# Optimization experiments

Hardware: AMD Instinct MI355X
Metric: run time of the kernel (lower is better)

Reference implementation:

```python
import jax, jax.numpy as jnp
import numpy as np

MP1, NX, P, HT, HE = 524288, 32768, 128, 128, 64


def setup_inputs() -> dict:
    key = jax.random.key(0)
    ks = jax.random.split(key, 12)
    w = lambda k, shape, fan_in: jax.random.normal(k, shape, jnp.float32) / np.sqrt(fan_in).astype(np.float32)
    a = jax.random.normal(ks[0], (MP1,), jnp.float32)
    x = jax.random.uniform(ks[1], (NX,), jnp.float32)
    t = jax.random.uniform(ks[2], (), jnp.float32)
    # DeepONet-style operator net: branch Linear(Mp1 -> p), trunk MLP (x,t) -> p
    Wb = w(ks[3], (P, MP1), MP1); bb = jnp.zeros((P,), jnp.float32)
    Wt1 = w(ks[4], (HT, 2), 2); bt1 = jnp.zeros((HT,), jnp.float32)
    Wt2 = w(ks[5], (HT, HT), HT); bt2 = jnp.zeros((HT,), jnp.float32)
    Wt3 = w(ks[6], (P, HT), HT); bt3 = jnp.zeros((P,), jnp.float32)
    # EnergyNet F(y,z): tiny smooth MLP R^2 -> R (needs 3rd-order derivatives)
    We1 = w(ks[7], (HE, 2), 2); be1 = jnp.zeros((HE,), jnp.float32)
    We2 = w(ks[8], (HE, HE), HE); be2 = jnp.zeros((HE,), jnp.float32)
    We3 = w(ks[9], (1, HE), HE); be3 = jnp.zeros((1,), jnp.float32)
    return dict(a=a, x=x, t=t, Wb=Wb, bb=bb, Wt1=Wt1, bt1=bt1, Wt2=Wt2, bt2=bt2,
                Wt3=Wt3, bt3=bt3, We1=We1, be1=be1, We2=We2, be2=be2, We3=We3, be3=be3)


def reference(a, x, t, Wb, bb, Wt1, bt1, Wt2, bt2, Wt3, bt3, We1, be1, We2, be2, We3, be3):
    # branch encoding of the input function a: (P,)
    b = Wb @ a + bb

    def u_fn(xi):  # scalar x -> scalar u(x, t)
        h = jnp.tanh(Wt1 @ jnp.stack([xi, t]) + bt1)
        h = jnp.tanh(Wt2 @ h + bt2)
        return jnp.dot(b, Wt3 @ h + bt3)

    def F(y, z):  # EnergyNet: scalar (y, z) -> scalar
        h = jnp.tanh(We1 @ jnp.stack([y, z]) + be1)
        h = jnp.tanh(We2 @ h + be2)
        return (We3 @ h + be3)[0]

    # u and its spatial derivatives, vmapped over the Nx grid points
    u = jax.vmap(u_fn)(x)
    u_x = jax.vmap(jax.grad(u_fn))(x)
    u_xx = jax.vmap(jax.grad(jax.grad(u_fn)))(x)
    u_xxx = jax.vmap(jax.grad(jax.grad(jax.grad(u_fn))))(x)

    # all needed partials of F(y, z), exactly as in the original module
    F_y = jax.grad(F)
    F_yz = jax.vmap(jax.grad(F_y, 1))(u, u_x)
    F_yy, F_yyz = jax.vmap(jax.value_and_grad(jax.grad(F_y), 1))(u, u_x)
    F_zz, (F_yzz, F_zzz) = jax.vmap(jax.value_and_grad(jax.grad(jax.grad(F, 1), 1), (0, 1)))(u, u_x)

    F_yx = F_yy * u_x + F_yz * u_xx
    F_zxx = (F_yz * u_xx + F_zz * u_xxx + F_yyz * u_x ** 2
             + 2.0 * F_yzz * u_x * u_xx + F_zzz * u_xx ** 2)
    return (-F_yx + F_zxx).reshape(x.shape[0])
```

## Files before the change

kernel.cpp:

```cpp
#include <hip/hip_runtime.h>
#include <cmath>

#define MP1 524288
#define NXP 32768


__global__ __launch_bounds__(256) void prep1_k(const float* __restrict__ Wt2,
                                               const float* __restrict__ We2,
                                               float* __restrict__ ws) {
    int idx = blockIdx.x * 256 + threadIdx.x;
    if (idx < 128) ws[idx] = 0.0f;
    if (idx < 16384) {
        int j = idx >> 7, k = idx & 127;
        ws[512 + k * 128 + j] = Wt2[idx];
    }
    if (idx < 4096) {
        int m = idx >> 6, i = idx & 63;
        ws[16896 + i * 64 + m] = We2[idx];
    }
}

__global__ __launch_bounds__(256) void gemv_k(const float* __restrict__ Wb,
                                              const float* __restrict__ a,
                                              float* __restrict__ b_acc) {
    const int row = blockIdx.y;
    const int chunk = blockIdx.x;
    const int t = threadIdx.x;
    size_t base = (size_t)row * MP1 + (size_t)chunk * 16384;
    const float4* W4 = (const float4*)(Wb + base);
    const float4* A4 = (const float4*)(a + (size_t)chunk * 16384);
    float sum = 0.0f;
#pragma unroll
    for (int it = 0; it < 16; ++it) {
        float4 w = W4[t + it * 256];
        float4 av = A4[t + it * 256];
        sum += w.x * av.x + w.y * av.y + w.z * av.z + w.w * av.w;
    }
#pragma unroll
    for (int off = 32; off > 0; off >>= 1) sum += __shfl_down(sum, off, 64);
    __shared__ float red[4];
    int wid = t >> 6;
    if ((t & 63) == 0) red[wid] = sum;
    __syncthreads();
    if (t == 0) atomicAdd(&b_acc[row], red[0] + red[1] + red[2] + red[3]);
}

__global__ __launch_bounds__(128) void prep2_k(const float* __restrict__ ws_in,
                                               const float* __restrict__ bb,
                                               const float* __restrict__ Wt3,
                                               const float* __restrict__ bt3,
                                               float* __restrict__ ws) {
    int k = threadIdx.x;
    float cv = 0.0f;
    for (int j = 0; j < 128; ++j)
        cv = fmaf(ws_in[j] + bb[j], Wt3[j * 128 + k], cv);
    ws[128 + k] = cv;
    float p = (ws_in[k] + bb[k]) * bt3[k];
#pragma unroll
    for (int off = 32; off > 0; off >>= 1) p += __shfl_down(p, off, 64);
    __shared__ float red[2];
    if ((k & 63) == 0) red[k >> 6] = p;
    __syncthreads();
    if (k == 0) ws[256] = red[0] + red[1];
}

#define H1V 0
#define RED 8192
#define URED 10240
#define FRED 10496
#define LDSF 13568

__global__ __launch_bounds__(512, 4) void point_k(const float* __restrict__ x,
                                                  const float* __restrict__ tptr,
                                                  const float* __restrict__ Wt1,
                                                  const float* __restrict__ bt1,
                                                  const float* __restrict__ bt2,
                                                  const float* __restrict__ We1,
                                                  const float* __restrict__ be1,
                                                  const float* __restrict__ be2,
                                                  const float* __restrict__ We3,
                                                  const float* __restrict__ ws,
                                                  float* __restrict__ out) {
    __shared__ float lds[LDSF];
    const int tid = threadIdx.x;
    const int p = tid & 63;
    const int slice = __builtin_amdgcn_readfirstlane(tid >> 6);
    const int i = blockIdx.x * 64 + p;
    const float xi = x[i];
    const float tt = tptr[0];
    const float* __restrict__ cvec = ws + 128;
    const float* __restrict__ WT2t = ws + 512;
    const float* __restrict__ WE2t = ws + 16896;
    const float u_const = ws[256];

#pragma unroll
    for (int q = 0; q < 16; ++q) {
        int k = slice * 16 + q;
        float z = fmaf(Wt1[2 * k], xi, fmaf(Wt1[2 * k + 1], tt, bt1[k]));
        lds[H1V + k * 64 + p] = tanhf(z);
    }
    __syncthreads();

    {
        float a0[16], a1[16], a2[16], a3[16];
#pragma unroll
        for (int jj = 0; jj < 16; ++jj) { a0[jj] = 0.f; a1[jj] = 0.f; a2[jj] = 0.f; a3[jj] = 0.f; }
#pragma unroll 2
        for (int k = 0; k < 128; ++k) {
            float v = lds[H1V + k * 64 + p];
            float w = Wt1[2 * k];
            float s = 1.f - v * v;
            float f2 = -2.f * v * s;
            float f3 = 2.f * s * (2.f * v * v - s);
            float d1 = s * w;
            float d2 = f2 * w * w;
            float d3 = f3 * w * w * w;
            const float* wrow = WT2t + k * 128 + slice * 16;
#pragma unroll
            for (int jj = 0; jj < 16; ++jj) {
                float wjk = wrow[jj];
                a0[jj] = fmaf(wjk, v, a0[jj]);
                a1[jj] = fmaf(wjk, d1, a1[jj]);
                a2[jj] = fmaf(wjk, d2, a2[jj]);
                a3[jj] = fmaf(wjk, d3, a3[jj]);
            }
        }
        float u0 = 0.f, u1 = 0.f, u2 = 0.f, u3 = 0.f;
#pragma unroll
        for (int jj = 0; jj < 16; ++jj) {
            int j = slice * 16 + jj;
            float z0 = a0[jj] + bt2[j];
            float z1 = a1[jj], z2 = a2[jj], z3 = a3[jj];
            float v = tanhf(z0);
            float s = 1.f - v * v;
            float f2 = -2.f * v * s;
            float f3 = 2.f * s * (2.f * v * v - s);
            float cj = cvec[j];
            u0 = fmaf(cj, v, u0);
            u1 = fmaf(cj, s * z1, u1);
            u2 = fmaf(cj, f2 * z1 * z1 + s * z2, u2);
            u3 = fmaf(cj, f3 * z1 * z1 * z1 + 3.f * f2 * z1 * z2 + s * z3, u3);
        }
        float* r = lds + RED + (slice * 64 + p) * 4;
        r[0] = u0; r[1] = u1; r[2] = u2; r[3] = u3;
    }
    __syncthreads();

    if (tid < 64) {
        float u0 = u_const, u1 = 0.f, u2 = 0.f, u3 = 0.f;
#pragma unroll
        for (int s = 0; s < 8; ++s) {
            const float* r = lds + RED + (s * 64 + tid) * 4;
            u0 += r[0]; u1 += r[1]; u2 += r[2]; u3 += r[3];
        }
        float* u = lds + URED + tid * 4;
        u[0] = u0; u[1] = u1; u[2] = u2; u[3] = u3;
    }
    __syncthreads();

    const float y = lds[URED + p * 4 + 0];
    const float z = lds[URED + p * 4 + 1];

#pragma unroll
    for (int q = 0; q < 8; ++q) {
        int ii = slice * 8 + q;
        float g = fmaf(We1[2 * ii], y, fmaf(We1[2 * ii + 1], z, be1[ii]));
        lds[H1V + ii * 64 + p] = tanhf(g);
    }
    __syncthreads();

    {
        float A0[8], A1[8], A2[8], A3[8], A4[8], A5[8], A6[8], A7[8], A8[8];
#pragma unroll
        for (int mm = 0; mm < 8; ++mm) {
            A0[mm] = 0.f; A1[mm] = 0.f; A2[mm] = 0.f; A3[mm] = 0.f; A4[mm] = 0.f;
            A5[mm] = 0.f; A6[mm] = 0.f; A7[mm] = 0.f; A8[mm] = 0.f;
        }
#pragma unroll 2
        for (int ii = 0; ii < 64; ++ii) {
            float v = lds[H1V + ii * 64 + p];
            float w0 = We1[2 * ii], w1 = We1[2 * ii + 1];
            float s = 1.f - v * v;
            float f2 = -2.f * v * s;
            float f3 = 2.f * s * (2.f * v * v - s);
            float j1 = s * w0, j2 = s * w1;
            float j3 = f2 * w0 * w0, j4 = f2 * w0 * w1, j5 = f2 * w1 * w1;
            float j6 = f3 * w0 * w0 * w1, j7 = f3 * w0 * w1 * w1, j8 = f3 * w1 * w1 * w1;
            const float* wrow = WE2t + ii * 64 + slice * 8;
#pragma unroll
            for (int mm = 0; mm < 8; ++mm) {
                float wmi = wrow[mm];
                A0[mm] = fmaf(wmi, v,  A0[mm]);
                A1[mm] = fmaf(wmi, j1, A1[mm]);
                A2[mm] = fmaf(wmi, j2, A2[mm]);
                A3[mm] = fmaf(wmi, j3, A3[mm]);
                A4[mm] = fmaf(wmi, j4, A4[mm]);
                A5[mm] = fmaf(wmi, j5, A5[mm]);
                A6[mm] = fmaf(wmi, j6, A6[mm]);
                A7[mm] = fmaf(wmi, j7, A7[mm]);
                A8[mm] = fmaf(wmi, j8, A8[mm]);
            }
        }
        float Fyy = 0.f, Fyz = 0.f, Fzz = 0.f, Fyyz = 0.f, Fyzz = 0.f, Fzzz = 0.f;
#pragma unroll
        for (int mm = 0; mm < 8; ++mm) {
            int m = slice * 8 + mm;
            float G0 = A0[mm] + be2[m];
            float v = tanhf(G0);
            float s = 1.f - v * v;
            float f2 = -2.f * v * s;
            float f3 = 2.f * s * (2.f * v * v - s);
            float Gy = A1[mm], Gz = A2[mm];
            float Gyy = A3[mm], Gyz = A4[mm], Gzz = A5[mm];
            float Hyy = f2 * Gy * Gy + s * Gyy;
            float Hyz = f2 * Gy * Gz + s * Gyz;
            float Hzz = f2 * Gz * Gz + s * Gzz;
            float Hyyz = f3 * Gy * Gy * Gz + f2 * (Gyy * Gz + 2.f * Gyz * Gy) + s * A6[mm];
            float Hyzz = f3 * Gy * Gz * Gz + f2 * (2.f * Gyz * Gz + Gzz * Gy) + s * A7[mm];
            float Hzzz = f3 * Gz * Gz * Gz + 3.f * f2 * Gzz * Gz + s * A8[mm];
            float w3 = We3[m];
            Fyy  = fmaf(w3, Hyy,  Fyy);
            Fyz  = fmaf(w3, Hyz,  Fyz);
            Fzz  = fmaf(w3, Hzz,  Fzz);
            Fyyz = fmaf(w3, Hyyz, Fyyz);
            Fyzz = fmaf(w3, Hyzz, Fyzz);
            Fzzz = fmaf(w3, Hzzz, Fzzz);
        }
        float* r = lds + FRED + (slice * 64 + p) * 6;
        r[0] = Fyy; r[1] = Fyz; r[2] = Fzz; r[3] = Fyyz; r[4] = Fyzz; r[5] = Fzzz;
    }
    __syncthreads();

    if (tid < 64) {
        float F[6] = {0.f, 0.f, 0.f, 0.f, 0.f, 0.f};
#pragma unroll
        for (int s = 0; s < 8; ++s) {
            const float* r = lds + FRED + (s * 64 + tid) * 6;
#pragma unroll
            for (int q = 0; q < 6; ++q) F[q] += r[q];
        }
        const float* u = lds + URED + tid * 4;
        float u1 = u[1], u2 = u[2], u3 = u[3];
        float F_yx  = F[0] * u1 + F[1] * u2;
        float F_zxx = F[1] * u2 + F[2] * u3 + F[3] * u1 * u1
                    + 2.f * F[4] * u1 * u2 + F[5] * u2 * u2;
        out[blockIdx.x * 64 + tid] = F_zxx - F_yx;
    }
}

extern "C" void kernel_launch(void* const* d_in, const int* in_sizes, int n_in,
                              void* d_out, int out_size, void* d_ws, size_t ws_size,
                              hipStream_t stream) {
    const float* a   = (const float*)d_in[0];
    const float* x   = (const float*)d_in[1];
    const float* t   = (const float*)d_in[2];
    const float* Wb  = (const float*)d_in[3];
    const float* bb  = (const float*)d_in[4];
    const float* Wt1 = (const float*)d_in[5];
    const float* bt1 = (const float*)d_in[6];
    const float* Wt2 = (const float*)d_in[7];
    const float* bt2 = (const float*)d_in[8];
    const float* Wt3 = (const float*)d_in[9];
    const float* bt3 = (const float*)d_in[10];
    const float* We1 = (const float*)d_in[11];
    const float* be1 = (const float*)d_in[12];
    const float* We2 = (const float*)d_in[13];
    const float* be2 = (const float*)d_in[14];
    const float* We3 = (const float*)d_in[15];

    float* ws = (float*)d_ws;
    float* out = (float*)d_out;

    prep1_k<<<64, 256, 0, stream>>>(Wt2, We2, ws);
    gemv_k<<<dim3(32, 128), 256, 0, stream>>>(Wb, a, ws);
    prep2_k<<<1, 128, 0, stream>>>(ws, bb, Wt3, bt3, ws);
    point_k<<<NXP / 64, 512, 0, stream>>>(x, t, Wt1, bt1, bt2, We1, be1, be2, We3,
                                          ws, out);
}
```

Before: 493.9 us.

## Stage point-kernel weights in LDS and stream GEMV weights with nontemporal loads

```diff
diff --git a/kernel.cpp b/kernel.cpp
--- a/kernel.cpp
+++ b/kernel.cpp
@@ -3,6 +3,8 @@
 
 #define MP1 524288
 #define NXP 32768
+
+typedef float vfloat4 __attribute__((ext_vector_type(4)));
 
 
 __global__ __launch_bounds__(256) void prep1_k(const float* __restrict__ Wt2,
@@ -23,18 +25,18 @@
 __global__ __launch_bounds__(256) void gemv_k(const float* __restrict__ Wb,
                                               const float* __restrict__ a,
                                               float* __restrict__ b_acc) {
-    const int row = blockIdx.y;
-    const int chunk = blockIdx.x;
+    const int row = blockIdx.x;
+    const int chunk = blockIdx.y;
     const int t = threadIdx.x;
     size_t base = (size_t)row * MP1 + (size_t)chunk * 16384;
-    const float4* W4 = (const float4*)(Wb + base);
+    const vfloat4* W4 = (const vfloat4*)(Wb + base);
     const float4* A4 = (const float4*)(a + (size_t)chunk * 16384);
     float sum = 0.0f;
 #pragma unroll
     for (int it = 0; it < 16; ++it) {
-        float4 w = W4[t + it * 256];
+        vfloat4 w = __builtin_nontemporal_load(&W4[t + it * 256]);
         float4 av = A4[t + it * 256];
-        sum += w.x * av.x + w.y * av.y + w.z * av.z + w.w * av.w;
+        sum += w[0] * av.x + w[1] * av.y + w[2] * av.z + w[3] * av.w;
     }
 #pragma unroll
     for (int off = 32; off > 0; off >>= 1) sum += __shfl_down(sum, off, 64);
@@ -64,11 +66,19 @@
     if (k == 0) ws[256] = red[0] + red[1];
 }
 
-#define H1V 0
-#define RED 8192
-#define URED 10240
-#define FRED 10496
-#define LDSF 13568
+#define SW_WT1 0
+#define SW_BT1 256
+#define SW_BT2 384
+#define SW_CVEC 512
+#define SW_WE1 640
+#define SW_BE1 768
+#define SW_BE2 832
+#define SW_WE3 896
+#define UREDP 960
+#define H1V_ 1216
+#define FREDP (H1V_ + 4096)
+#define SCR_ 9408
+#define LDSF 13504
 
 __global__ __launch_bounds__(512, 4) void point_k(const float* __restrict__ x,
                                                   const float* __restrict__ tptr,
@@ -81,115 +91,155 @@
                                                   const float* __restrict__ We3,
                                                   const float* __restrict__ ws,
                                                   float* __restrict__ out) {
-    __shared__ float lds[LDSF];
+    __shared__ __align__(16) float lds[LDSF];
     const int tid = threadIdx.x;
     const int p = tid & 63;
     const int slice = __builtin_amdgcn_readfirstlane(tid >> 6);
     const int i = blockIdx.x * 64 + p;
     const float xi = x[i];
     const float tt = tptr[0];
-    const float* __restrict__ cvec = ws + 128;
-    const float* __restrict__ WT2t = ws + 512;
-    const float* __restrict__ WE2t = ws + 16896;
     const float u_const = ws[256];
+
+    if (tid < 256) lds[SW_WT1 + tid] = Wt1[tid];
+    else if (tid < 384) lds[SW_BT1 + tid - 256] = bt1[tid - 256];
+    else lds[SW_BT2 + tid - 384] = bt2[tid - 384];
+    {
+        int o = 512 + tid;
+        if (o < 640) lds[o] = ws[128 + (o - 512)];
+        else if (o < 768) lds[o] = We1[o - 640];
+        else if (o < 832) lds[o] = be1[o - 768];
+        else if (o < 896) lds[o] = be2[o - 832];
+        else if (o < 960) lds[o] = We3[o - 896];
+    }
+    __syncthreads();
 
 #pragma unroll
     for (int q = 0; q < 16; ++q) {
         int k = slice * 16 + q;
-        float z = fmaf(Wt1[2 * k], xi, fmaf(Wt1[2 * k + 1], tt, bt1[k]));
-        lds[H1V + k * 64 + p] = tanhf(z);
-    }
-    __syncthreads();
-
-    {
-        float a0[16], a1[16], a2[16], a3[16];
-#pragma unroll
-        for (int jj = 0; jj < 16; ++jj) { a0[jj] = 0.f; a1[jj] = 0.f; a2[jj] = 0.f; a3[jj] = 0.f; }
+        float z = fmaf(lds[SW_WT1 + 2 * k], xi,
+                       fmaf(lds[SW_WT1 + 2 * k + 1], tt, lds[SW_BT1 + k]));
+        lds[H1V_ + k * 64 + p] = tanhf(z);
+    }
+
+    float a0[16], a1[16], a2[16], a3[16];
+#pragma unroll
+    for (int jj = 0; jj < 16; ++jj) { a0[jj] = 0.f; a1[jj] = 0.f; a2[jj] = 0.f; a3[jj] = 0.f; }
+    for (int c = 0; c < 4; ++c) {
+        __syncthreads();
+        {
+            const float4* src = (const float4*)(ws + 512 + c * 4096);
+            float4* dst = (float4*)(lds + SCR_);
+            dst[tid] = src[tid];
+            dst[tid + 512] = src[tid + 512];
+        }
+        __syncthreads();
 #pragma unroll 2
-        for (int k = 0; k < 128; ++k) {
-            float v = lds[H1V + k * 64 + p];
-            float w = Wt1[2 * k];
+        for (int kl = 0; kl < 32; ++kl) {
+            int k = c * 32 + kl;
+            float v = lds[H1V_ + k * 64 + p];
+            float w = lds[SW_WT1 + 2 * k];
             float s = 1.f - v * v;
             float f2 = -2.f * v * s;
             float f3 = 2.f * s * (2.f * v * v - s);
+            float w2 = w * w;
             float d1 = s * w;
-            float d2 = f2 * w * w;
-            float d3 = f3 * w * w * w;
-            const float* wrow = WT2t + k * 128 + slice * 16;
+            float d2 = f2 * w2;
+            float d3 = f3 * w2 * w;
+            const float4* wr = (const float4*)(lds + SCR_ + kl * 128 + slice * 16);
+            float4 wv0 = wr[0], wv1 = wr[1], wv2 = wr[2], wv3 = wr[3];
+            const float wf[16] = {wv0.x, wv0.y, wv0.z, wv0.w, wv1.x, wv1.y, wv1.z, wv1.w,
+                                  wv2.x, wv2.y, wv2.z, wv2.w, wv3.x, wv3.y, wv3.z, wv3.w};
 #pragma unroll
             for (int jj = 0; jj < 16; ++jj) {
-                float wjk = wrow[jj];
+                float wjk = wf[jj];
                 a0[jj] = fmaf(wjk, v, a0[jj]);
                 a1[jj] = fmaf(wjk, d1, a1[jj]);
                 a2[jj] = fmaf(wjk, d2, a2[jj]);
                 a3[jj] = fmaf(wjk, d3, a3[jj]);
             }
         }
-        float u0 = 0.f, u1 = 0.f, u2 = 0.f, u3 = 0.f;
-#pragma unroll
-        for (int jj = 0; jj < 16; ++jj) {
-            int j = slice * 16 + jj;
-            float z0 = a0[jj] + bt2[j];
-            float z1 = a1[jj], z2 = a2[jj], z3 = a3[jj];
-            float v = tanhf(z0);
+    }
+    float u0 = 0.f, u1 = 0.f, u2 = 0.f, u3 = 0.f;
+#pragma unroll
+    for (int jj = 0; jj < 16; ++jj) {
+        int j = slice * 16 + jj;
+        float z0 = a0[jj] + lds[SW_BT2 + j];
+        float z1 = a1[jj], z2 = a2[jj], z3 = a3[jj];
+        float v = tanhf(z0);
+        float s = 1.f - v * v;
+        float f2 = -2.f * v * s;
+        float f3 = 2.f * s * (2.f * v * v - s);
+        float cj = lds[SW_CVEC + j];
+        u0 = fmaf(cj, v, u0);
+        u1 = fmaf(cj, s * z1, u1);
+        u2 = fmaf(cj, f2 * z1 * z1 + s * z2, u2);
+        u3 = fmaf(cj, f3 * z1 * z1 * z1 + 3.f * f2 * z1 * z2 + s * z3, u3);
+    }
+    __syncthreads();
+    lds[SCR_ + 0 * 512 + slice * 64 + p] = u0;
+    lds[SCR_ + 1 * 512 + slice * 64 + p] = u1;
+    lds[SCR_ + 2 * 512 + slice * 64 + p] = u2;
+    lds[SCR_ + 3 * 512 + slice * 64 + p] = u3;
+    __syncthreads();
+
+    if (tid < 64) {
+        float r0 = u_const, r1 = 0.f, r2 = 0.f, r3 = 0.f;
+#pragma unroll
+        for (int s = 0; s < 8; ++s) {
+            r0 += lds[SCR_ + 0 * 512 + s * 64 + tid];
+            r1 += lds[SCR_ + 1 * 512 + s * 64 + tid];
+            r2 += lds[SCR_ + 2 * 512 + s * 64 + tid];
+            r3 += lds[SCR_ + 3 * 512 + s * 64 + tid];
+        }
+        lds[UREDP + 0 * 64 + tid] = r0;
+        lds[UREDP + 1 * 64 + tid] = r1;
+        lds[UREDP + 2 * 64 + tid] = r2;
+        lds[UREDP + 3 * 64 + tid] = r3;
+    }
+    __syncthreads();
+
+    {
+        const float4* src = (const float4*)(ws + 16896);
+        float4* dst = (float4*)(lds + SCR_);
+        dst[tid] = src[tid];
+        dst[tid + 512] = src[tid + 512];
+    }
+    const float y = lds[UREDP + 0 * 64 + p];
+    const float z = lds[UREDP + 1 * 64 + p];
+#pragma unroll
+    for (int q = 0; q < 8; ++q) {
+        int ii = slice * 8 + q;
+        float g = fmaf(lds[SW_WE1 + 2 * ii], y,
+                       fmaf(lds[SW_WE1 + 2 * ii + 1], z, lds[SW_BE1 + ii]));
+        lds[H1V_ + ii * 64 + p] = tanhf(g);
+    }
+    __syncthreads();
+
+    {
+        float A0[8], A1[8], A2[8], A3[8], A4[8], A5[8], A6[8], A7[8], A8[8];
+#pragma unroll
+        for (int mm = 0; mm < 8; ++mm) {
+            A0[mm] = 0.f; A1[mm] = 0.f; A2[mm] = 0.f; A3[mm] = 0.f; A4[mm] = 0.f;
+            A5[mm] = 0.f; A6[mm] = 0.f; A7[mm] = 0.f; A8[mm] = 0.f;
+        }
+#pragma unroll 2
+        for (int ii = 0; ii < 64; ++ii) {
+            float v = lds[H1V_ + ii * 64 + p];
+            float w0 = lds[SW_WE1 + 2 * ii];
+            float w1 = lds[SW_WE1 + 2 * ii + 1];
             float s = 1.f - v * v;
             float f2 = -2.f * v * s;
             float f3 = 2.f * s * (2.f * v * v - s);
-            float cj = cvec[j];
-            u0 = fmaf(cj, v, u0);
-            u1 = fmaf(cj, s * z1, u1);
-            u2 = fmaf(cj, f2 * z1 * z1 + s * z2, u2);
-            u3 = fmaf(cj, f3 * z1 * z1 * z1 + 3.f * f2 * z1 * z2 + s * z3, u3);
-        }
-        float* r = lds + RED + (slice * 64 + p) * 4;
-        r[0] = u0; r[1] = u1; r[2] = u2; r[3] = u3;
-    }
-    __syncthreads();
-
-    if (tid < 64) {
-        float u0 = u_const, u1 = 0.f, u2 = 0.f, u3 = 0.f;
-#pragma unroll
-        for (int s = 0; s < 8; ++s) {
-            const float* r = lds + RED + (s * 64 + tid) * 4;
-            u0 += r[0]; u1 += r[1]; u2 += r[2]; u3 += r[3];
-        }
-        float* u = lds + URED + tid * 4;
-        u[0] = u0; u[1] = u1; u[2] = u2; u[3] = u3;
-    }
-    __syncthreads();
-
-    const float y = lds[URED + p * 4 + 0];
-    const float z = lds[URED + p * 4 + 1];
-
-#pragma unroll
-    for (int q = 0; q < 8; ++q) {
-        int ii = slice * 8 + q;
-        float g = fmaf(We1[2 * ii], y, fmaf(We1[2 * ii + 1], z, be1[ii]));
-        lds[H1V + ii * 64 + p] = tanhf(g);
-    }
-    __syncthreads();
-
-    {
-        float A0[8], A1[8], A2[8], A3[8], A4[8], A5[8], A6[8], A7[8], A8[8];
-#pragma unroll
-        for (int mm = 0; mm < 8; ++mm) {
-            A0[mm] = 0.f; A1[mm] = 0.f; A2[mm] = 0.f; A3[mm] = 0.f; A4[mm] = 0.f;
-            A5[mm] = 0.f; A6[mm] = 0.f; A7[mm] = 0.f; A8[mm] = 0.f;
-        }
-#pragma unroll 2
-        for (int ii = 0; ii < 64; ++ii) {
-            float v = lds[H1V + ii * 64 + p];
-            float w0 = We1[2 * ii], w1 = We1[2 * ii + 1];
-            float s = 1.f - v * v;
-            float f2 = -2.f * v * s;
-            float f3 = 2.f * s * (2.f * v * v - s);
+            float w00 = w0 * w0, w01 = w0 * w1, w11 = w1 * w1;
             float j1 = s * w0, j2 = s * w1;
-            float j3 = f2 * w0 * w0, j4 = f2 * w0 * w1, j5 = f2 * w1 * w1;
-            float j6 = f3 * w0 * w0 * w1, j7 = f3 * w0 * w1 * w1, j8 = f3 * w1 * w1 * w1;
-            const float* wrow = WE2t + ii * 64 + slice * 8;
+            float j3 = f2 * w00, j4 = f2 * w01, j5 = f2 * w11;
+            float j6 = f3 * w00 * w1, j7 = f3 * w01 * w1, j8 = f3 * w11 * w1;
+            const float4* wr = (const float4*)(lds + SCR_ + ii * 64 + slice * 8);
+            float4 wv0 = wr[0], wv1 = wr[1];
+            const float wf[8] = {wv0.x, wv0.y, wv0.z, wv0.w, wv1.x, wv1.y, wv1.z, wv1.w};
 #pragma unroll
             for (int mm = 0; mm < 8; ++mm) {
-                float wmi = wrow[mm];
+                float wmi = wf[mm];
                 A0[mm] = fmaf(wmi, v,  A0[mm]);
                 A1[mm] = fmaf(wmi, j1, A1[mm]);
                 A2[mm] = fmaf(wmi, j2, A2[mm]);
@@ -205,7 +255,7 @@
 #pragma unroll
         for (int mm = 0; mm < 8; ++mm) {
             int m = slice * 8 + mm;
-            float G0 = A0[mm] + be2[m];
+            float G0 = A0[mm] + lds[SW_BE2 + m];
             float v = tanhf(G0);
             float s = 1.f - v * v;
             float f2 = -2.f * v * s;
@@ -218,7 +268,7 @@
             float Hyyz = f3 * Gy * Gy * Gz + f2 * (Gyy * Gz + 2.f * Gyz * Gy) + s * A6[mm];
             float Hyzz = f3 * Gy * Gz * Gz + f2 * (2.f * Gyz * Gz + Gzz * Gy) + s * A7[mm];
             float Hzzz = f3 * Gz * Gz * Gz + 3.f * f2 * Gzz * Gz + s * A8[mm];
-            float w3 = We3[m];
+            float w3 = lds[SW_WE3 + m];
             Fyy  = fmaf(w3, Hyy,  Fyy);
             Fyz  = fmaf(w3, Hyz,  Fyz);
             Fzz  = fmaf(w3, Hzz,  Fzz);
@@ -226,8 +276,12 @@
             Fyzz = fmaf(w3, Hyzz, Fyzz);
             Fzzz = fmaf(w3, Hzzz, Fzzz);
         }
-        float* r = lds + FRED + (slice * 64 + p) * 6;
-        r[0] = Fyy; r[1] = Fyz; r[2] = Fzz; r[3] = Fyyz; r[4] = Fyzz; r[5] = Fzzz;
+        lds[FREDP + 0 * 512 + slice * 64 + p] = Fyy;
+        lds[FREDP + 1 * 512 + slice * 64 + p] = Fyz;
+        lds[FREDP + 2 * 512 + slice * 64 + p] = Fzz;
+        lds[FREDP + 3 * 512 + slice * 64 + p] = Fyyz;
+        lds[FREDP + 4 * 512 + slice * 64 + p] = Fyzz;
+        lds[FREDP + 5 * 512 + slice * 64 + p] = Fzzz;
     }
     __syncthreads();
 
@@ -235,15 +289,15 @@
         float F[6] = {0.f, 0.f, 0.f, 0.f, 0.f, 0.f};
 #pragma unroll
         for (int s = 0; s < 8; ++s) {
-            const float* r = lds + FRED + (s * 64 + tid) * 6;
-#pragma unroll
-            for (int q = 0; q < 6; ++q) F[q] += r[q];
-        }
-        const float* u = lds + URED + tid * 4;
-        float u1 = u[1], u2 = u[2], u3 = u[3];
-        float F_yx  = F[0] * u1 + F[1] * u2;
-        float F_zxx = F[1] * u2 + F[2] * u3 + F[3] * u1 * u1
-                    + 2.f * F[4] * u1 * u2 + F[5] * u2 * u2;
+#pragma unroll
+            for (int q = 0; q < 6; ++q) F[q] += lds[FREDP + q * 512 + s * 64 + tid];
+        }
+        float u1r = lds[UREDP + 1 * 64 + tid];
+        float u2r = lds[UREDP + 2 * 64 + tid];
+        float u3r = lds[UREDP + 3 * 64 + tid];
+        float F_yx  = F[0] * u1r + F[1] * u2r;
+        float F_zxx = F[1] * u2r + F[2] * u3r + F[3] * u1r * u1r
+                    + 2.f * F[4] * u1r * u2r + F[5] * u2r * u2r;
         out[blockIdx.x * 64 + tid] = F_zxx - F_yx;
     }
 }
@@ -272,7 +326,7 @@
     float* out = (float*)d_out;
 
     prep1_k<<<64, 256, 0, stream>>>(Wt2, We2, ws);
-    gemv_k<<<dim3(32, 128), 256, 0, stream>>>(Wb, a, ws);
+    gemv_k<<<dim3(128, 32), 256, 0, stream>>>(Wb, a, ws);
     prep2_k<<<1, 128, 0, stream>>>(ws, bb, Wt3, bt3, ws);
     point_k<<<NXP / 64, 512, 0, stream>>>(x, t, Wt1, bt1, bt2, We1, be1, be2, We3,
                                           ws, out);
```

New measurement: 473.8 us. 1.04x faster.
